# Performance work log

Measured on AMD Instinct MI355X. Metric: run time of the kernel, lower is better.

## Reference

```python
import jax, jax.numpy as jnp
import numpy as np
import math

L = 2          # num_layers
H = 1024       # hidden_dim
NH = 16        # num_heads
HD = H // NH   # head_dim = 64
M = 4096       # mlp_dim
GRIDS = [(2, 32, 32), (1, 32, 32)]  # (t,h,w) per image -> 2048 + 1024 = 3072 tokens
THETA = 10000.0
EPS = 1e-5


def _rope_cos_sin(grids, head_dim):
    # Rope2DPosEmbRepeated: interleaved (x,y) complex rotations, repeated over t.
    n = head_dim // 4
    freqs = 1.0 / (THETA ** (np.arange(0, head_dim, 4, dtype=np.float64)[:n] / head_dim))
    parts = []
    for t, h, w in grids:
        ys, xs = np.meshgrid(np.arange(h), np.arange(w), indexing='ij')
        xa = xs.reshape(-1, 1).astype(np.float64) * freqs  # [h*w, n]
        ya = ys.reshape(-1, 1).astype(np.float64) * freqs
        ang = np.stack([xa, ya], axis=-1).reshape(-1, head_dim // 2)  # interleave x,y
        parts.append(np.tile(ang, (t, 1)))
    ang = np.concatenate(parts, axis=0).astype(np.float32)  # [S, head_dim//2]
    return jnp.asarray(np.cos(ang)), jnp.asarray(np.sin(ang))


def _segment_ids(grids):
    lens = [t * h * w for t, h, w in grids]
    return jnp.asarray(np.repeat(np.arange(len(lens)), lens))


def _layernorm(x, g, b):
    mu = jnp.mean(x, axis=-1, keepdims=True)
    var = jnp.mean(jnp.square(x - mu), axis=-1, keepdims=True)
    return (x - mu) * jax.lax.rsqrt(var + EPS) * g + b


def _apply_rope(x, cos, sin):
    # x: [S, NH, HD]; cos/sin: [S, HD//2] -> broadcast over heads (unsqueeze(-2))
    xr = x.reshape(x.shape[0], x.shape[1], HD // 2, 2)
    a, b = xr[..., 0], xr[..., 1]
    c = cos[:, None, :]
    s = sin[:, None, :]
    oa = a * c - b * s
    ob = a * s + b * c
    return jnp.stack([oa, ob], axis=-1).reshape(x.shape)


def setup_inputs() -> dict:
    key = jax.random.key(0)
    ks = jax.random.split(key, 8)
    S = sum(t * h * w for t, h, w in GRIDS)
    sH = 1.0 / math.sqrt(H)
    sM = 1.0 / math.sqrt(M)
    return {
        'hidden_states': jax.random.normal(ks[0], (S, H), jnp.float32),
        'grid_thws': jnp.asarray(np.array(GRIDS, dtype=np.int32)),
        'ln0_g': jnp.ones((L, H), jnp.float32),
        'ln0_b': jnp.zeros((L, H), jnp.float32),
        'wqkv': jax.random.normal(ks[1], (L, 3 * H, H), jnp.float32) * sH,
        'wo': jax.random.normal(ks[2], (L, H, H), jnp.float32) * sH,
        'ln1_g': jnp.ones((L, H), jnp.float32),
        'ln1_b': jnp.zeros((L, H), jnp.float32),
        'fc0_w': jax.random.normal(ks[3], (L, M, H), jnp.float32) * math.sqrt(2.0 / H),
        'fc0_b': jnp.zeros((L, M), jnp.float32),
        'fc1_w': jax.random.normal(ks[4], (L, H, M), jnp.float32) * math.sqrt(2.0 / M),
        'fc1_b': jnp.zeros((L, H), jnp.float32),
        'fln_g': jnp.ones((H,), jnp.float32),
        'fln_b': jnp.zeros((H,), jnp.float32),
    }


def reference(hidden_states, grid_thws, ln0_g, ln0_b, wqkv, wo, ln1_g, ln1_b,
              fc0_w, fc0_b, fc1_w, fc1_b, fln_g, fln_b):
    grids = [tuple(int(v) for v in row) for row in np.asarray(grid_thws)]
    S = hidden_states.shape[0]
    cos, sin = _rope_cos_sin(grids, HD)
    seg = _segment_ids(grids)
    mask = seg[:, None] == seg[None, :]  # block-diagonal [S, S]
    scale = 1.0 / math.sqrt(HD)

    x = hidden_states
    for i in range(L):
        h = _layernorm(x, ln0_g[i], ln0_b[i])
        qkv = (h @ wqkv[i].T).reshape(S, 3, NH, HD)
        q, k, v = qkv[:, 0], qkv[:, 1], qkv[:, 2]
        q = _apply_rope(q, cos, sin)
        k = _apply_rope(k, cos, sin)
        scores = jnp.einsum('qhd,khd->hqk', q, k) * scale
        scores = jnp.where(mask[None], scores, -1e30)
        attn = jax.nn.softmax(scores, axis=-1)
        o = jnp.einsum('hqk,khd->qhd', attn, v).reshape(S, H)
        x = x + o @ wo[i].T
        h2 = _layernorm(x, ln1_g[i], ln1_b[i])
        mlp = jax.nn.gelu(h2 @ fc0_w[i].T + fc0_b[i], approximate=False) @ fc1_w[i].T + fc1_b[i]
        x = x + mlp
    return _layernorm(x, fln_g, fln_b)
```

## Files before the change

### kernel.cpp

```cpp
#include <hip/hip_runtime.h>
#include <hip/hip_bf16.h>
#include <cstdint>
#include <math.h>

constexpr int ST   = 3072;
constexpr int HH   = 1024;
constexpr int NHD  = 16;
constexpr int DH   = 64;
constexpr int MMLP = 4096;
constexpr int SEG0 = 2048;

using short8 = __attribute__((ext_vector_type(8))) short;
using f32x4  = __attribute__((ext_vector_type(4))) float;

#if __has_builtin(__builtin_amdgcn_exp2f)
#define EXP2F __builtin_amdgcn_exp2f
#else
#define EXP2F exp2f
#endif

#if __has_builtin(__builtin_amdgcn_rcpf)
#define RCPF __builtin_amdgcn_rcpf
#else
#define RCPF(x) (1.f / (x))
#endif

__device__ __forceinline__ unsigned short f2bf(float f) {
  unsigned int u = __float_as_uint(f);
  u += 0x7fffu + ((u >> 16) & 1u);
  return (unsigned short)(u >> 16);
}

__device__ __forceinline__ void g2l16(const void* g, void* l) {
  __builtin_amdgcn_global_load_lds(
      (const __attribute__((address_space(1))) unsigned int*)g,
      (__attribute__((address_space(3))) unsigned int*)l, 16, 0, 0);
}

__device__ __forceinline__ float erf_fast(float z) {
  const float az = fabsf(z);
  const float t1 = RCPF(1.f + 0.3275911f * az);
  const float poly =
      t1 * (0.254829592f +
            t1 * (-0.284496736f +
                  t1 * (1.421413741f +
                        t1 * (-1.453152027f + t1 * 1.061405429f))));
  const float e = EXP2F(-az * az * 1.4426950408889634f);
  const float v = 1.f - poly * e;
  return (z < 0.f) ? -v : v;
}

__global__ void f32_to_bf16(const float* __restrict__ src,
                            unsigned short* __restrict__ dst, int n4) {
  const int i = blockIdx.x * blockDim.x + threadIdx.x;
  if (i >= n4) return;
  const float4 v = ((const float4*)src)[i];
  ushort4 u;
  u.x = f2bf(v.x); u.y = f2bf(v.y); u.z = f2bf(v.z); u.w = f2bf(v.w);
  ((ushort4*)dst)[i] = u;
}

__global__ void ln_kernel(const float* __restrict__ x,
                          const float* __restrict__ g,
                          const float* __restrict__ b,
                          unsigned short* obf) {
  const int s = blockIdx.x;
  const int t = threadIdx.x;
  const float4 v = ((const float4*)(x + (size_t)s * HH))[t];
  float s1 = v.x + v.y + v.z + v.w;
  float s2 = v.x * v.x + v.y * v.y + v.z * v.z + v.w * v.w;
#pragma unroll
  for (int off = 32; off > 0; off >>= 1) {
    s1 += __shfl_down(s1, off);
    s2 += __shfl_down(s2, off);
  }
  __shared__ float red[8];
  __shared__ float stat[2];
  const int wv = t >> 6, ln = t & 63;
  if (ln == 0) { red[wv] = s1; red[4 + wv] = s2; }
  __syncthreads();
  if (t == 0) {
    float a1 = red[0] + red[1] + red[2] + red[3];
    float a2 = red[4] + red[5] + red[6] + red[7];
    float mu = a1 * (1.f / HH);
    float var = a2 * (1.f / HH) - mu * mu;
    stat[0] = mu;
    stat[1] = rsqrtf(var + 1e-5f);
  }
  __syncthreads();
  const float mu = stat[0], rs = stat[1];
  const float4 gg = ((const float4*)g)[t];
  const float4 bb = ((const float4*)b)[t];
  ushort4 u;
  u.x = f2bf((v.x - mu) * rs * gg.x + bb.x);
  u.y = f2bf((v.y - mu) * rs * gg.y + bb.y);
  u.z = f2bf((v.z - mu) * rs * gg.z + bb.z);
  u.w = f2bf((v.w - mu) * rs * gg.w + bb.w);
  ((ushort4*)(obf + (size_t)s * HH))[t] = u;
}

template <int NS>
__global__ void ln_comb(const float* __restrict__ xin,
                        const float* __restrict__ P,
                        const float* __restrict__ bias,
                        const float* __restrict__ g,
                        const float* __restrict__ b,
                        float* __restrict__ xout,
                        unsigned short* obf, float* of) {
  const int s = blockIdx.x;
  const int t = threadIdx.x;
  const size_t row = (size_t)s * HH;
  const size_t sl = (size_t)ST * HH;
  float4 v = ((const float4*)(xin + row))[t];
#pragma unroll
  for (int c = 0; c < NS; ++c) {
    const float4 p = ((const float4*)(P + c * sl + row))[t];
    v.x += p.x; v.y += p.y; v.z += p.z; v.w += p.w;
  }
  if (bias) {
    const float4 bb4 = ((const float4*)bias)[t];
    v.x += bb4.x; v.y += bb4.y; v.z += bb4.z; v.w += bb4.w;
  }
  if (xout) ((float4*)(xout + row))[t] = v;
  float s1 = v.x + v.y + v.z + v.w;
  float s2 = v.x * v.x + v.y * v.y + v.z * v.z + v.w * v.w;
#pragma unroll
  for (int off = 32; off > 0; off >>= 1) {
    s1 += __shfl_down(s1, off);
    s2 += __shfl_down(s2, off);
  }
  __shared__ float red[8];
  __shared__ float stat[2];
  const int wv = t >> 6, ln = t & 63;
  if (ln == 0) { red[wv] = s1; red[4 + wv] = s2; }
  __syncthreads();
  if (t == 0) {
    float a1 = red[0] + red[1] + red[2] + red[3];
    float a2 = red[4] + red[5] + red[6] + red[7];
    float mu = a1 * (1.f / HH);
    float var = a2 * (1.f / HH) - mu * mu;
    stat[0] = mu;
    stat[1] = rsqrtf(var + 1e-5f);
  }
  __syncthreads();
  const float mu = stat[0], rs = stat[1];
  const float4 gg = ((const float4*)g)[t];
  const float4 bb = ((const float4*)b)[t];
  float4 o;
  o.x = (v.x - mu) * rs * gg.x + bb.x;
  o.y = (v.y - mu) * rs * gg.y + bb.y;
  o.z = (v.z - mu) * rs * gg.z + bb.z;
  o.w = (v.w - mu) * rs * gg.w + bb.w;
  if (obf) {
    ushort4 u;
    u.x = f2bf(o.x); u.y = f2bf(o.y); u.z = f2bf(o.z); u.w = f2bf(o.w);
    ((ushort4*)(obf + row))[t] = u;
  } else {
    ((float4*)(of + row))[t] = o;
  }
}

__global__ void rope_tables(float* __restrict__ cosb, float* __restrict__ sinb) {
  const int s = blockIdx.x;
  const int j = threadIdx.x;
  const int p = (s < SEG0) ? (s & 1023) : (s - SEG0);
  const int pos = (j & 1) ? (p >> 5) : (p & 31);
  const int f = j >> 1;
  const double freq = pow(10000.0, -(double)f / 16.0);
  const double ang = (double)pos * freq;
  cosb[s * 32 + j] = (float)cos(ang);
  sinb[s * 32 + j] = (float)sin(ang);
}

__global__ void v_transpose(const unsigned short* __restrict__ Vb,
                            unsigned short* __restrict__ VT) {
  const int h = blockIdx.y;
  const int s0 = blockIdx.x * 64;
  const int tid = threadIdx.x;
  __shared__ unsigned short T[64][72];
  const int tr = tid >> 3, pc = tid & 7;
#pragma unroll
  for (int it = 0; it < 2; ++it) {
    short8 v = *(const short8*)(Vb + (size_t)(s0 + it * 32 + tr) * HH + h * DH + pc * 8);
    *(short8*)&T[it * 32 + tr][pc * 8] = v;
  }
  __syncthreads();
  const int d = tid >> 2;
  const int c0 = (tid & 3) * 16;
  short8 o0, o1;
#pragma unroll
  for (int j = 0; j < 8; ++j) { o0[j] = T[c0 + j][d]; o1[j] = T[c0 + 8 + j][d]; }
  unsigned short* dst = VT + (size_t)(h * 64 + d) * ST + s0 + c0;
  *(short8*)dst = o0;
  *(short8*)(dst + 8) = o1;
}

template <int MODE>
__launch_bounds__(256)
__global__ void gemm_bt(const unsigned short* __restrict__ A,
                        const unsigned short* __restrict__ B,
                        float* Cf, unsigned short* Cb,
                        const float* __restrict__ bias,
                        const float* __restrict__ bias2,
                        int N, int K) {
  __shared__ unsigned short Al[128 * 64];
  __shared__ unsigned short Bl[128 * 64];
  const int tid = threadIdx.x;
  const int lane = tid & 63;
  const int wave = tid >> 6;
  const int col = lane & 15;
  const int quad = lane >> 4;
  const int m0 = blockIdx.y * 128;
  const int n0 = blockIdx.x * 128;
  const int wm = (wave & 1) * 64;
  const int wn = (wave >> 1) * 64;

  int kFrom = 0, kTo = K;
  if (MODE == 4) {
    const int kc = K / gridDim.z;
    kFrom = blockIdx.z * kc;
    kTo = kFrom + kc;
  }

  f32x4 acc[4][4] = {};

  const int tr = tid >> 3;
  const int pb = tid & 7;
  const int kb = pb ^ (tr & 7);
  const unsigned short* Ag = A + (size_t)(m0 + tr) * K + kb * 8;
  const unsigned short* Bg = B + (size_t)(n0 + tr) * K + kb * 8;
  unsigned short* Alw = Al + (size_t)tid * 8;
  unsigned short* Blw = Bl + (size_t)tid * 8;

  for (int k0 = kFrom; k0 < kTo; k0 += 64) {
#pragma unroll
    for (int it = 0; it < 4; ++it) {
      g2l16(Ag + (size_t)(it * 32) * K + k0, Alw + it * 2048);
      g2l16(Bg + (size_t)(it * 32) * K + k0, Blw + it * 2048);
    }
    __syncthreads();
#pragma unroll
    for (int kk = 0; kk < 2; ++kk) {
      short8 af[4], bfr[4];
#pragma unroll
      for (int mt = 0; mt < 4; ++mt) {
        int r = wm + mt * 16 + col;
        int kp = (kk * 4 + quad) ^ (r & 7);
        af[mt] = *(const short8*)(Al + r * 64 + kp * 8);
      }
#pragma unroll
      for (int nt = 0; nt < 4; ++nt) {
        int r = wn + nt * 16 + col;
        int kp = (kk * 4 + quad) ^ (r & 7);
        bfr[nt] = *(const short8*)(Bl + r * 64 + kp * 8);
      }
#pragma unroll
      for (int mt = 0; mt < 4; ++mt)
#pragma unroll
        for (int nt = 0; nt < 4; ++nt)
          acc[mt][nt] = __builtin_amdgcn_mfma_f32_16x16x32_bf16(
              af[mt], bfr[nt], acc[mt][nt], 0, 0, 0);
    }
    __syncthreads();
  }
  const size_t zoff = (MODE == 4) ? (size_t)blockIdx.z * ST * N : 0;
  const int bufsel = (MODE == 5) ? (n0 >> 10) : 0;
  const float SQ = 0.125f * 1.4426950408889634f;
#pragma unroll
  for (int mt = 0; mt < 4; ++mt) {
#pragma unroll
    for (int r = 0; r < 4; ++r) {
      const int gr = m0 + wm + mt * 16 + quad * 4 + r;
#pragma unroll
      for (int nt = 0; nt < 4; ++nt) {
        const int gc = n0 + wn + nt * 16 + col;
        const float v = acc[mt][nt][r];
        if (MODE == 2) {
          const float tt = v + bias[gc];
          const float gl = 0.5f * tt * (1.f + erf_fast(tt * 0.70710678f));
          Cb[(size_t)gr * N + gc] = f2bf(gl);
        } else if (MODE == 4) {
          Cf[zoff + (size_t)gr * N + gc] = v;
        } else {
          const int c1023 = gc & 1023;
          unsigned short* out = Cb + (size_t)bufsel * (ST * HH);
          if (bufsel == 2) {
            out[(size_t)gr * HH + c1023] = f2bf(v);
          } else {
            const int j = (c1023 & 63) >> 1;
            const float cs = bias[gr * 32 + j];
            const float sn = bias2[gr * 32 + j];
            const float vp = __shfl_xor(v, 1);
            float res = (lane & 1) ? (vp * sn + v * cs) : (v * cs - vp * sn);
            if (bufsel == 0) res *= SQ;
            out[(size_t)gr * HH + c1023] = f2bf(res);
          }
        }
      }
    }
  }
}

__launch_bounds__(256)
__global__ void attn_flash(const unsigned short* __restrict__ Qb,
                           const unsigned short* __restrict__ Kb,
                           const unsigned short* __restrict__ VT,
                           float* __restrict__ Op01,
                           float* __restrict__ Op23,
                           float* __restrict__ lbuf) {
  const int h = blockIdx.y;
  const int unit = blockIdx.x;
  int qt, chunk, s0;
  if (unit < 64) { qt = unit >> 2; chunk = unit & 3; s0 = 0; }
  else { const int v = unit - 64; qt = 16 + (v >> 1); chunk = v & 1; s0 = SEG0; }
  const int q0 = qt * 128;
  const int koff = s0 + chunk * 512;

  const int tid = threadIdx.x;
  const int lane = tid & 63;
  const int wave = tid >> 6;
  const int col = lane & 15;
  const int quad = lane >> 4;

  __shared__ unsigned short Kl[128 * 64];
  __shared__ unsigned short Vl[64 * 128];
  __shared__ unsigned int Pl[4][2][2][16][20];

  short8 qf[2][2];
#pragma unroll
  for (int mt = 0; mt < 2; ++mt) {
    const unsigned short* qrow =
        Qb + (size_t)(q0 + wave * 32 + mt * 16 + col) * HH + h * DH;
    qf[mt][0] = *(const short8*)(qrow + quad * 8);
    qf[mt][1] = *(const short8*)(qrow + 32 + quad * 8);
  }

  short8 ones;
#pragma unroll
  for (int j = 0; j < 8; ++j) ones[j] = (short)0x3F80;

  f32x4 accO[2][4] = {};
  f32x4 accL[2] = {};
  const float SHIFT = 16.f;

  const int trK = tid >> 3, pbK = tid & 7;
  const int kbK = pbK ^ (trK & 7);
  const int trV = tid >> 4, pbV = tid & 15;

  for (int kb0 = 0; kb0 < 512; kb0 += 128) {
#pragma unroll
    for (int it = 0; it < 4; ++it)
      g2l16(Kb + (size_t)(koff + kb0 + it * 32 + trK) * HH + h * DH + kbK * 8,
            (unsigned short*)Kl + it * 2048 + (size_t)tid * 8);
#pragma unroll
    for (int it = 0; it < 4; ++it) {
      const int d = it * 16 + trV;
      const int kbv = pbV ^ (d & 7);
      g2l16(VT + (size_t)(h * 64 + d) * ST + koff + kb0 + kbv * 8,
            (unsigned short*)Vl + it * 2048 + (size_t)tid * 8);
    }
    __syncthreads();

    f32x4 sc[2][8];
#pragma unroll
    for (int nt = 0; nt < 8; ++nt) {
      const int r = nt * 16 + col;
      const short8 kf0 = *(const short8*)(Kl + r * 64 + ((quad) ^ (r & 7)) * 8);
      const short8 kf1 = *(const short8*)(Kl + r * 64 + ((4 + quad) ^ (r & 7)) * 8);
#pragma unroll
      for (int mt = 0; mt < 2; ++mt) {
        f32x4 z = {};
        z = __builtin_amdgcn_mfma_f32_16x16x32_bf16(kf0, qf[mt][0], z, 0, 0, 0);
        sc[mt][nt] = __builtin_amdgcn_mfma_f32_16x16x32_bf16(kf1, qf[mt][1], z, 0, 0, 0);
      }
    }

#pragma unroll
    for (int kd = 0; kd < 4; ++kd) {
      const int par = kd & 1;
#pragma unroll
      for (int mt = 0; mt < 2; ++mt) {
#pragma unroll
        for (int ntl = 0; ntl < 2; ++ntl) {
          const f32x4 s4 = sc[mt][kd * 2 + ntl];
          const float p0 = EXP2F(s4[0] - SHIFT);
          const float p1 = EXP2F(s4[1] - SHIFT);
          const float p2 = EXP2F(s4[2] - SHIFT);
          const float p3 = EXP2F(s4[3] - SHIFT);
          uint2 w;
          w.x = (unsigned)f2bf(p0) | ((unsigned)f2bf(p1) << 16);
          w.y = (unsigned)f2bf(p2) | ((unsigned)f2bf(p3) << 16);
          *(uint2*)&Pl[wave][par][mt][col][ntl * 8 + quad * 2] = w;
        }
      }
      short8 pf[2];
#pragma unroll
      for (int mt = 0; mt < 2; ++mt)
        pf[mt] = *(const short8*)&Pl[wave][par][mt][col][quad * 4];
#pragma unroll
      for (int mt = 0; mt < 2; ++mt)
        accL[mt] = __builtin_amdgcn_mfma_f32_16x16x32_bf16(pf[mt], ones,
                                                           accL[mt], 0, 0, 0);
#pragma unroll
      for (int dt = 0; dt < 4; ++dt) {
        const int rv = dt * 16 + col;
        const int pbv2 = (kd * 4 + quad) ^ (rv & 7);
        const short8 vf = *(const short8*)(Vl + rv * 128 + pbv2 * 8);
#pragma unroll
        for (int mt = 0; mt < 2; ++mt)
          accO[mt][dt] = __builtin_amdgcn_mfma_f32_16x16x32_bf16(
              pf[mt], vf, accO[mt][dt], 0, 0, 0);
      }
    }
    __syncthreads();
  }

  float* Op = (chunk < 2) ? (Op01 + (size_t)chunk * (ST * HH))
                          : (Op23 + (size_t)(chunk - 2) * (ST * HH));
#pragma unroll
  for (int mt = 0; mt < 2; ++mt)
#pragma unroll
    for (int r = 0; r < 4; ++r) {
      const int row = q0 + wave * 32 + mt * 16 + quad * 4 + r;
#pragma unroll
      for (int dt = 0; dt < 4; ++dt)
        Op[(size_t)row * HH + h * DH + dt * 16 + col] = accO[mt][dt][r];
      if (col == 0)
        lbuf[((size_t)chunk * ST + row) * NHD + h] = accL[mt][r];
    }
}

__global__ void attn_combine(const float* __restrict__ Op01,
                             const float* __restrict__ Op23,
                             const float* __restrict__ lbuf,
                             unsigned short* __restrict__ out) {
  const int s = blockIdx.x;
  const int t = threadIdx.x;
  const int h = t >> 4;
  const int d0 = (t & 15) * 4;
  const int nc = (s < SEG0) ? 4 : 2;
  float L = 0.f;
  float4 o = make_float4(0.f, 0.f, 0.f, 0.f);
  for (int c = 0; c < nc; ++c) {
    L += lbuf[((size_t)c * ST + s) * NHD + h];
    const float* Op = (c < 2) ? (Op01 + (size_t)c * (ST * HH))
                              : (Op23 + (size_t)(c - 2) * (ST * HH));
    const float4 v = *(const float4*)(Op + (size_t)s * HH + h * DH + d0);
    o.x += v.x; o.y += v.y; o.z += v.z; o.w += v.w;
  }
  const float inv = 1.f / L;
  ushort4 u;
  u.x = f2bf(o.x * inv); u.y = f2bf(o.y * inv);
  u.z = f2bf(o.z * inv); u.w = f2bf(o.w * inv);
  ((ushort4*)(out + (size_t)s * HH))[t] = u;
}

extern "C" void kernel_launch(void* const* d_in, const int* in_sizes, int n_in,
                              void* d_out, int out_size, void* d_ws, size_t ws_size,
                              hipStream_t stream) {
  const float* hs   = (const float*)d_in[0];
  const float* ln0g = (const float*)d_in[2];
  const float* ln0b = (const float*)d_in[3];
  const float* wqkv = (const float*)d_in[4];
  const float* wo   = (const float*)d_in[5];
  const float* ln1g = (const float*)d_in[6];
  const float* ln1b = (const float*)d_in[7];
  const float* fc0w = (const float*)d_in[8];
  const float* fc0b = (const float*)d_in[9];
  const float* fc1w = (const float*)d_in[10];
  const float* fc1b = (const float*)d_in[11];
  const float* flng = (const float*)d_in[12];
  const float* flnb = (const float*)d_in[13];

  char* ws = (char*)d_ws;
  unsigned short* wqkv_bf = (unsigned short*)(ws + 0);
  unsigned short* wo_bf   = (unsigned short*)(ws + 12582912);
  unsigned short* fc0_bf  = (unsigned short*)(ws + 16777216);
  unsigned short* fc1_bf  = (unsigned short*)(ws + 33554432);
  float*          x       = (float*)(ws + 50331648);
  unsigned short* abf     = (unsigned short*)(ws + 62914560);
  unsigned short* gelu_bf = (unsigned short*)(ws + 69206016);
  unsigned short* Qbf     = (unsigned short*)(ws + 132120576);
  unsigned short* Kbf     = (unsigned short*)(ws + 138412032);
  unsigned short* Vbf     = (unsigned short*)(ws + 144703488);
  float*          cosb    = (float*)(ws + 150994944);
  float*          sinb    = (float*)(ws + 151388160);
  unsigned short* VT    = (unsigned short*)(ws + 94371840);
  float*          Op01  = (float*)(ws + 100663296);
  float*          Op23  = (float*)(ws + 69206016);
  float*          lbuf  = (float*)(ws + 144703488);
  float*          Pbuf  = (float*)(ws + 94371840);

  f32_to_bf16<<<6144, 256, 0, stream>>>(wqkv, wqkv_bf, 1572864);
  f32_to_bf16<<<2048, 256, 0, stream>>>(wo, wo_bf, 524288);
  f32_to_bf16<<<8192, 256, 0, stream>>>(fc0w, fc0_bf, 2097152);
  f32_to_bf16<<<8192, 256, 0, stream>>>(fc1w, fc1_bf, 2097152);
  rope_tables<<<ST, 32, 0, stream>>>(cosb, sinb);

  for (int i = 0; i < 2; ++i) {
    if (i == 0)
      ln_kernel<<<ST, 256, 0, stream>>>(hs, ln0g, ln0b, abf);
    gemm_bt<5><<<dim3(24, 24), 256, 0, stream>>>(
        abf, wqkv_bf + (size_t)i * 3 * HH * HH, nullptr, Qbf, cosb, sinb,
        3 * HH, HH);
    v_transpose<<<dim3(48, 16), 256, 0, stream>>>(Vbf, VT);
    attn_flash<<<dim3(80, 16), 256, 0, stream>>>(Qbf, Kbf, VT, Op01, Op23, lbuf);
    attn_combine<<<ST, 256, 0, stream>>>(Op01, Op23, lbuf, abf);
    gemm_bt<4><<<dim3(8, 24, 2), 256, 0, stream>>>(
        abf, wo_bf + (size_t)i * HH * HH, Pbuf, nullptr, nullptr, nullptr,
        HH, HH);
    ln_comb<2><<<ST, 256, 0, stream>>>(
        (i == 0) ? hs : x, Pbuf, nullptr, ln1g + i * HH, ln1b + i * HH,
        x, abf, nullptr);
    gemm_bt<2><<<dim3(32, 24), 256, 0, stream>>>(
        abf, fc0_bf + (size_t)i * MMLP * HH, nullptr, gelu_bf, fc0b + i * MMLP,
        nullptr, MMLP, HH);
    gemm_bt<4><<<dim3(8, 24, 2), 256, 0, stream>>>(
        gelu_bf, fc1_bf + (size_t)i * HH * MMLP, Pbuf, nullptr, nullptr,
        nullptr, HH, MMLP);
    if (i == 0)
      ln_comb<2><<<ST, 256, 0, stream>>>(x, Pbuf, fc1b, ln0g + HH, ln0b + HH,
                                         x, abf, nullptr);
    else
      ln_comb<2><<<ST, 256, 0, stream>>>(x, Pbuf, fc1b + HH, flng, flnb,
                                         nullptr, nullptr, (float*)d_out);
  }
}
```

Baseline: 640.9 us.

## Fuse V transpose into QKV epilogue, halve attention splits, merge weight casts

The QKV GEMM epilogue now writes V already transposed into VT, which removes the separate v_transpose kernel. Q/K RoPE outputs are stored as paired 32-bit writes, with cos/sin read from one interleaved float2 table. The four weight-cast launches become a single cast_all kernel. Attention splits keys into 1024-wide chunks (2 for the first segment, 1 for the second), halving the partial buffers the combine step reads but also halving the attention grid to 640 blocks, which may lower occupancy.

```diff
diff --git a/kernel.cpp b/kernel.cpp
--- a/kernel.cpp
+++ b/kernel.cpp
@@ -50,14 +50,22 @@
   return (z < 0.f) ? -v : v;
 }
 
-__global__ void f32_to_bf16(const float* __restrict__ src,
-                            unsigned short* __restrict__ dst, int n4) {
+__global__ void cast_all(const float* __restrict__ s0,
+                         const float* __restrict__ s1,
+                         const float* __restrict__ s2,
+                         const float* __restrict__ s3,
+                         ushort4* __restrict__ dst) {
   const int i = blockIdx.x * blockDim.x + threadIdx.x;
-  if (i >= n4) return;
-  const float4 v = ((const float4*)src)[i];
+  const float4* src;
+  int off;
+  if (i < 1572864)      { src = (const float4*)s0; off = i; }
+  else if (i < 2097152) { src = (const float4*)s1; off = i - 1572864; }
+  else if (i < 4194304) { src = (const float4*)s2; off = i - 2097152; }
+  else                  { src = (const float4*)s3; off = i - 4194304; }
+  const float4 v = src[off];
   ushort4 u;
   u.x = f2bf(v.x); u.y = f2bf(v.y); u.z = f2bf(v.z); u.w = f2bf(v.w);
-  ((ushort4*)dst)[i] = u;
+  dst[i] = u;
 }
 
 __global__ void ln_kernel(const float* __restrict__ x,
@@ -160,7 +168,7 @@
   }
 }
 
-__global__ void rope_tables(float* __restrict__ cosb, float* __restrict__ sinb) {
+__global__ void rope_tables(float2* __restrict__ cs2) {
   const int s = blockIdx.x;
   const int j = threadIdx.x;
   const int p = (s < SEG0) ? (s & 1023) : (s - SEG0);
@@ -168,31 +176,7 @@
   const int f = j >> 1;
   const double freq = pow(10000.0, -(double)f / 16.0);
   const double ang = (double)pos * freq;
-  cosb[s * 32 + j] = (float)cos(ang);
-  sinb[s * 32 + j] = (float)sin(ang);
-}
-
-__global__ void v_transpose(const unsigned short* __restrict__ Vb,
-                            unsigned short* __restrict__ VT) {
-  const int h = blockIdx.y;
-  const int s0 = blockIdx.x * 64;
-  const int tid = threadIdx.x;
-  __shared__ unsigned short T[64][72];
-  const int tr = tid >> 3, pc = tid & 7;
-#pragma unroll
-  for (int it = 0; it < 2; ++it) {
-    short8 v = *(const short8*)(Vb + (size_t)(s0 + it * 32 + tr) * HH + h * DH + pc * 8);
-    *(short8*)&T[it * 32 + tr][pc * 8] = v;
-  }
-  __syncthreads();
-  const int d = tid >> 2;
-  const int c0 = (tid & 3) * 16;
-  short8 o0, o1;
-#pragma unroll
-  for (int j = 0; j < 8; ++j) { o0[j] = T[c0 + j][d]; o1[j] = T[c0 + 8 + j][d]; }
-  unsigned short* dst = VT + (size_t)(h * 64 + d) * ST + s0 + c0;
-  *(short8*)dst = o0;
-  *(short8*)(dst + 8) = o1;
+  cs2[s * 32 + j] = make_float2((float)cos(ang), (float)sin(ang));
 }
 
 template <int MODE>
@@ -201,7 +185,6 @@
                         const unsigned short* __restrict__ B,
                         float* Cf, unsigned short* Cb,
                         const float* __restrict__ bias,
-                        const float* __restrict__ bias2,
                         int N, int K) {
   __shared__ unsigned short Al[128 * 64];
   __shared__ unsigned short Bl[128 * 64];
@@ -263,9 +246,56 @@
     }
     __syncthreads();
   }
+
+  if (MODE == 5) {
+    const int bufsel = n0 >> 10;
+    if (bufsel == 2) {
+      unsigned short* vt = (unsigned short*)Cf;
+#pragma unroll
+      for (int mt = 0; mt < 4; ++mt) {
+        const int gr0 = m0 + wm + mt * 16 + quad * 4;
+#pragma unroll
+        for (int nt = 0; nt < 4; ++nt) {
+          const int gc = (n0 + wn + nt * 16 + col) & 1023;
+          ushort4 u;
+          u.x = f2bf(acc[mt][nt][0]);
+          u.y = f2bf(acc[mt][nt][1]);
+          u.z = f2bf(acc[mt][nt][2]);
+          u.w = f2bf(acc[mt][nt][3]);
+          *(ushort4*)(vt + (size_t)gc * ST + gr0) = u;
+        }
+      }
+    } else {
+      const float2* tab = (const float2*)bias;
+      unsigned short* out = Cb + (size_t)bufsel * (ST * HH);
+      const float SQ = 0.125f * 1.4426950408889634f;
+#pragma unroll
+      for (int mt = 0; mt < 4; ++mt) {
+#pragma unroll
+        for (int r = 0; r < 4; ++r) {
+          const int gr = m0 + wm + mt * 16 + quad * 4 + r;
+#pragma unroll
+          for (int nt = 0; nt < 4; ++nt) {
+            const int gc = n0 + wn + nt * 16 + col;
+            const int c1023 = gc & 1023;
+            const int j = (c1023 & 63) >> 1;
+            const float2 cs = tab[gr * 32 + j];
+            const float v = acc[mt][nt][r];
+            const float vp = __shfl_xor(v, 1);
+            float res = (lane & 1) ? (vp * cs.y + v * cs.x)
+                                   : (v * cs.x - vp * cs.y);
+            if (bufsel == 0) res *= SQ;
+            const float rp = __shfl_xor(res, 1);
+            if (!(lane & 1))
+              *(unsigned int*)(out + (size_t)gr * HH + c1023) =
+                  (unsigned)f2bf(res) | ((unsigned)f2bf(rp) << 16);
+          }
+        }
+      }
+    }
+    return;
+  }
   const size_t zoff = (MODE == 4) ? (size_t)blockIdx.z * ST * N : 0;
-  const int bufsel = (MODE == 5) ? (n0 >> 10) : 0;
-  const float SQ = 0.125f * 1.4426950408889634f;
 #pragma unroll
   for (int mt = 0; mt < 4; ++mt) {
 #pragma unroll
@@ -279,22 +309,8 @@
           const float tt = v + bias[gc];
           const float gl = 0.5f * tt * (1.f + erf_fast(tt * 0.70710678f));
           Cb[(size_t)gr * N + gc] = f2bf(gl);
-        } else if (MODE == 4) {
+        } else {
           Cf[zoff + (size_t)gr * N + gc] = v;
-        } else {
-          const int c1023 = gc & 1023;
-          unsigned short* out = Cb + (size_t)bufsel * (ST * HH);
-          if (bufsel == 2) {
-            out[(size_t)gr * HH + c1023] = f2bf(v);
-          } else {
-            const int j = (c1023 & 63) >> 1;
-            const float cs = bias[gr * 32 + j];
-            const float sn = bias2[gr * 32 + j];
-            const float vp = __shfl_xor(v, 1);
-            float res = (lane & 1) ? (vp * sn + v * cs) : (v * cs - vp * sn);
-            if (bufsel == 0) res *= SQ;
-            out[(size_t)gr * HH + c1023] = f2bf(res);
-          }
         }
       }
     }
@@ -305,16 +321,15 @@
 __global__ void attn_flash(const unsigned short* __restrict__ Qb,
                            const unsigned short* __restrict__ Kb,
                            const unsigned short* __restrict__ VT,
-                           float* __restrict__ Op01,
-                           float* __restrict__ Op23,
+                           float* __restrict__ Op,
                            float* __restrict__ lbuf) {
   const int h = blockIdx.y;
   const int unit = blockIdx.x;
   int qt, chunk, s0;
-  if (unit < 64) { qt = unit >> 2; chunk = unit & 3; s0 = 0; }
-  else { const int v = unit - 64; qt = 16 + (v >> 1); chunk = v & 1; s0 = SEG0; }
+  if (unit < 32) { qt = unit >> 1; chunk = unit & 1; s0 = 0; }
+  else { qt = 16 + (unit - 32); chunk = 0; s0 = SEG0; }
   const int q0 = qt * 128;
-  const int koff = s0 + chunk * 512;
+  const int koff = s0 + chunk * 1024;
 
   const int tid = threadIdx.x;
   const int lane = tid & 63;
@@ -347,7 +362,7 @@
   const int kbK = pbK ^ (trK & 7);
   const int trV = tid >> 4, pbV = tid & 15;
 
-  for (int kb0 = 0; kb0 < 512; kb0 += 128) {
+  for (int kb0 = 0; kb0 < 1024; kb0 += 128) {
 #pragma unroll
     for (int it = 0; it < 4; ++it)
       g2l16(Kb + (size_t)(koff + kb0 + it * 32 + trK) * HH + h * DH + kbK * 8,
@@ -415,8 +430,7 @@
     __syncthreads();
   }
 
-  float* Op = (chunk < 2) ? (Op01 + (size_t)chunk * (ST * HH))
-                          : (Op23 + (size_t)(chunk - 2) * (ST * HH));
+  float* Opc = Op + (size_t)chunk * (ST * HH);
 #pragma unroll
   for (int mt = 0; mt < 2; ++mt)
 #pragma unroll
@@ -424,28 +438,26 @@
       const int row = q0 + wave * 32 + mt * 16 + quad * 4 + r;
 #pragma unroll
       for (int dt = 0; dt < 4; ++dt)
-        Op[(size_t)row * HH + h * DH + dt * 16 + col] = accO[mt][dt][r];
+        Opc[(size_t)row * HH + h * DH + dt * 16 + col] = accO[mt][dt][r];
       if (col == 0)
         lbuf[((size_t)chunk * ST + row) * NHD + h] = accL[mt][r];
     }
 }
 
-__global__ void attn_combine(const float* __restrict__ Op01,
-                             const float* __restrict__ Op23,
+__global__ void attn_combine(const float* __restrict__ Op,
                              const float* __restrict__ lbuf,
                              unsigned short* __restrict__ out) {
   const int s = blockIdx.x;
   const int t = threadIdx.x;
   const int h = t >> 4;
   const int d0 = (t & 15) * 4;
-  const int nc = (s < SEG0) ? 4 : 2;
+  const int nc = (s < SEG0) ? 2 : 1;
   float L = 0.f;
   float4 o = make_float4(0.f, 0.f, 0.f, 0.f);
   for (int c = 0; c < nc; ++c) {
     L += lbuf[((size_t)c * ST + s) * NHD + h];
-    const float* Op = (c < 2) ? (Op01 + (size_t)c * (ST * HH))
-                              : (Op23 + (size_t)(c - 2) * (ST * HH));
-    const float4 v = *(const float4*)(Op + (size_t)s * HH + h * DH + d0);
+    const float4 v =
+        *(const float4*)(Op + (size_t)c * (ST * HH) + (size_t)s * HH + h * DH + d0);
     o.x += v.x; o.y += v.y; o.z += v.z; o.w += v.w;
   }
   const float inv = 1.f / L;
@@ -469,8 +481,8 @@
   const float* fc0b = (const float*)d_in[9];
   const float* fc1w = (const float*)d_in[10];
   const float* fc1b = (const float*)d_in[11];
-  const float* flng = (const float*)d_in[12];
-  const float* flnb = (const float*)d_in[13];
+  const float* fln_g = (const float*)d_in[12];
+  const float* fln_b = (const float*)d_in[13];
 
   char* ws = (char*)d_ws;
   unsigned short* wqkv_bf = (unsigned short*)(ws + 0);
@@ -482,47 +494,39 @@
   unsigned short* gelu_bf = (unsigned short*)(ws + 69206016);
   unsigned short* Qbf     = (unsigned short*)(ws + 132120576);
   unsigned short* Kbf     = (unsigned short*)(ws + 138412032);
-  unsigned short* Vbf     = (unsigned short*)(ws + 144703488);
-  float*          cosb    = (float*)(ws + 150994944);
-  float*          sinb    = (float*)(ws + 151388160);
+  float*          cs2tab  = (float*)(ws + 150994944);
   unsigned short* VT    = (unsigned short*)(ws + 94371840);
-  float*          Op01  = (float*)(ws + 100663296);
-  float*          Op23  = (float*)(ws + 69206016);
+  float*          Op    = (float*)(ws + 100663296);
   float*          lbuf  = (float*)(ws + 144703488);
   float*          Pbuf  = (float*)(ws + 94371840);
 
-  f32_to_bf16<<<6144, 256, 0, stream>>>(wqkv, wqkv_bf, 1572864);
-  f32_to_bf16<<<2048, 256, 0, stream>>>(wo, wo_bf, 524288);
-  f32_to_bf16<<<8192, 256, 0, stream>>>(fc0w, fc0_bf, 2097152);
-  f32_to_bf16<<<8192, 256, 0, stream>>>(fc1w, fc1_bf, 2097152);
-  rope_tables<<<ST, 32, 0, stream>>>(cosb, sinb);
+  cast_all<<<24576, 256, 0, stream>>>(wqkv, wo, fc0w, fc1w, (ushort4*)ws);
+  rope_tables<<<ST, 32, 0, stream>>>((float2*)cs2tab);
 
   for (int i = 0; i < 2; ++i) {
     if (i == 0)
       ln_kernel<<<ST, 256, 0, stream>>>(hs, ln0g, ln0b, abf);
     gemm_bt<5><<<dim3(24, 24), 256, 0, stream>>>(
-        abf, wqkv_bf + (size_t)i * 3 * HH * HH, nullptr, Qbf, cosb, sinb,
+        abf, wqkv_bf + (size_t)i * 3 * HH * HH, (float*)VT, Qbf, cs2tab,
         3 * HH, HH);
-    v_transpose<<<dim3(48, 16), 256, 0, stream>>>(Vbf, VT);
-    attn_flash<<<dim3(80, 16), 256, 0, stream>>>(Qbf, Kbf, VT, Op01, Op23, lbuf);
-    attn_combine<<<ST, 256, 0, stream>>>(Op01, Op23, lbuf, abf);
+    attn_flash<<<dim3(40, 16), 256, 0, stream>>>(Qbf, Kbf, VT, Op, lbuf);
+    attn_combine<<<ST, 256, 0, stream>>>(Op, lbuf, abf);
     gemm_bt<4><<<dim3(8, 24, 2), 256, 0, stream>>>(
-        abf, wo_bf + (size_t)i * HH * HH, Pbuf, nullptr, nullptr, nullptr,
-        HH, HH);
+        abf, wo_bf + (size_t)i * HH * HH, Pbuf, nullptr, nullptr, HH, HH);
     ln_comb<2><<<ST, 256, 0, stream>>>(
         (i == 0) ? hs : x, Pbuf, nullptr, ln1g + i * HH, ln1b + i * HH,
         x, abf, nullptr);
     gemm_bt<2><<<dim3(32, 24), 256, 0, stream>>>(
         abf, fc0_bf + (size_t)i * MMLP * HH, nullptr, gelu_bf, fc0b + i * MMLP,
-        nullptr, MMLP, HH);
+        MMLP, HH);
     gemm_bt<4><<<dim3(8, 24, 2), 256, 0, stream>>>(
         gelu_bf, fc1_bf + (size_t)i * HH * MMLP, Pbuf, nullptr, nullptr,
-        nullptr, HH, MMLP);
+        HH, MMLP);
     if (i == 0)
       ln_comb<2><<<ST, 256, 0, stream>>>(x, Pbuf, fc1b, ln0g + HH, ln0b + HH,
                                          x, abf, nullptr);
     else
-      ln_comb<2><<<ST, 256, 0, stream>>>(x, Pbuf, fc1b + HH, flng, flnb,
+      ln_comb<2><<<ST, 256, 0, stream>>>(x, Pbuf, fc1b + HH, fln_g, fln_b,
                                          nullptr, nullptr, (float*)d_out);
   }
 }
```

Measured after the change: 618.9 us. -3.4%, faster.
